# Kernel tuning notes

Hardware: AMD Instinct MI355X
Metric: run time of the kernel (lower is better)

## Reference

```python
import jax, jax.numpy as jnp
import numpy as np

N, T, D, H = 16, 1024, 1024, 1024


def setup_inputs() -> dict:
    key = jax.random.key(0)
    ks = jax.random.split(key, 7)
    x = jax.random.normal(ks[0], (N, T, D), dtype=jnp.float32)
    reset = jax.random.randint(ks[1], (N, T), 0, 2).astype(bool)
    carry = jax.random.normal(ks[2], (N, T, H), dtype=jnp.float32)
    # learned parameters (orthogonal-ish init approximated by scaled gaussian)
    initial_h = jax.random.normal(ks[3], (H,), dtype=jnp.float32) * 0.1
    w_i = jax.random.normal(ks[4], (D, 3 * H), dtype=jnp.float32) * (1.0 / np.sqrt(D))
    w_h = jax.random.normal(ks[5], (H, 3 * H), dtype=jnp.float32) * (1.0 / np.sqrt(H))
    b = jnp.zeros((3 * H,), dtype=jnp.float32)
    return {"x": x, "reset": reset, "carry": carry,
            "initial_h": initial_h, "w_i": w_i, "w_h": w_h, "b": b}


def _gru_scan(x, reset, carry, initial_h, w_i, w_h, b):
    n, t, _ = x.shape
    h_dim = initial_h.shape[0]
    # learn_initial_h and not is_target: replace carry with learned init where reset
    init_b = jnp.broadcast_to(initial_h, (n, t, h_dim))
    carry = jnp.where(reset[..., None], init_b, carry)
    # precompute input projections for all timesteps (math-equivalent hoist)
    gx = jnp.einsum('ntd,dk->ntk', x, w_i)  # [N,T,3H]
    w_h_zr, w_h_a = w_h[:, :2 * h_dim], w_h[:, 2 * h_dim:]
    b_zr, b_a = b[:2 * h_dim], b[2 * h_dim:]

    def step(h, inp):
        gx_t, reset_t, carry_t = inp  # [N,3H], [N], [N,H]
        h = jnp.where(reset_t[:, None], carry_t, h)
        zr = jax.nn.sigmoid(gx_t[:, :2 * h_dim] + h @ w_h_zr + b_zr)
        z, r = zr[:, :h_dim], zr[:, h_dim:]
        a = jnp.tanh(gx_t[:, 2 * h_dim:] + (r * h) @ w_h_a + b_a)
        h_next = (1.0 - z) * h + z * a
        return h_next, h_next

    h0 = carry[:, 0, :]  # scan init is carry_seq[:1,:] per batch element
    _, hs = jax.lax.scan(step, h0, (gx.transpose(1, 0, 2), reset.T, carry.transpose(1, 0, 2)))
    states = hs.transpose(1, 0, 2)  # [N,T,H]
    return states


def reference(x, reset, carry, initial_h, w_i, w_h, b):
    states = _gru_scan(x, reset, carry, initial_h, w_i, w_h, b)
    # hk.GRU returns (next_state, next_state): outputs_seq == states_seq
    return states, states, initial_h[None, :]
```

## Files before the change

kernel.cpp:

```cpp
#include <hip/hip_runtime.h>

typedef __attribute__((ext_vector_type(8))) short s8v;
typedef __attribute__((ext_vector_type(4))) float f4v;
typedef __attribute__((ext_vector_type(4))) unsigned int u4v;
typedef unsigned long long u64;

__device__ __forceinline__ float bf2f(unsigned short u) {
    union { float f; unsigned int i; } v; v.i = ((unsigned int)u) << 16; return v.f;
}
__device__ __forceinline__ unsigned short f2bf(float f) {
    union { float f; unsigned int i; } v; v.f = f;
    unsigned int x = v.i;
    return (unsigned short)((x + 0x7fffu + ((x >> 16) & 1u)) >> 16);
}
__device__ __forceinline__ float ldf(const void* p, size_t i, int f32) {
    return f32 ? ((const float*)p)[i] : bf2f(((const unsigned short*)p)[i]);
}

__device__ __forceinline__ s8v ald16(u64* p) {
    union { s8v v; u64 u[2]; } r;
    r.u[0] = __hip_atomic_load(p,     __ATOMIC_RELAXED, __HIP_MEMORY_SCOPE_AGENT);
    r.u[1] = __hip_atomic_load(p + 1, __ATOMIC_RELAXED, __HIP_MEMORY_SCOPE_AGENT);
    return r.v;
}
__device__ __forceinline__ void pack_store64(u64* p, int lane, unsigned short val) {
    unsigned int mv = val;
    unsigned int lo = mv | (__shfl_down(mv, 16, 64) << 16);
    unsigned int hi = __shfl_down(mv, 32, 64) | (__shfl_down(mv, 48, 64) << 16);
    if (lane < 16) {
        u64 q = (u64)lo | ((u64)hi << 32);
        __hip_atomic_store(p, q, __ATOMIC_RELAXED, __HIP_MEMORY_SCOPE_AGENT);
    }
}

__device__ __forceinline__ void pollwait(int* f, int v) {
    while (__hip_atomic_load(f, __ATOMIC_RELAXED, __HIP_MEMORY_SCOPE_AGENT) < v)
        __builtin_amdgcn_s_sleep(1);
    __builtin_amdgcn_sched_barrier(0);
    asm volatile("" ::: "memory");
}

__global__ void detect_k(const unsigned short* __restrict__ xu,
                         const unsigned int* __restrict__ rw,
                         int* __restrict__ flags) {
    __shared__ int cnt;
    int tid = threadIdx.x;
    if (tid == 0) cnt = 0;
    for (int i = tid + 8; i < 528; i += 256) flags[i] = 0;
    __syncthreads();
    int bad = 0;
    for (int i = tid; i < 4096; i += 256) {
        unsigned short v = xu[i];
        int e = (v >> 7) & 0xFF;
        if (e == 0xFF || (e <= 90 && (v & 0x7FFFu) != 0)) bad++;
    }
    atomicAdd(&cnt, bad);
    __syncthreads();
    if (tid == 0) {
        flags[0] = (cnt > 16) ? 1 : 0;
        bool w01 = true, oddz = true, ones = false, b01 = true, h16 = true, fv = true;
        for (int i = 0; i < 32; ++i) {
            unsigned int w = rw[i];
            if (w > 1u) w01 = false;
            if ((i & 1) && w != 0u) oddz = false;
            if (w != 0u) ones = true;
            if ((w & 0xFFu) > 1u || ((w >> 8) & 0xFFu) > 1u ||
                ((w >> 16) & 0xFFu) > 1u || (w >> 24) > 1u) b01 = false;
            unsigned int lo = w & 0xFFFFu, hi = w >> 16;
            if (!((lo == 0u || lo == 0x3F80u) && (hi == 0u || hi == 0x3F80u))) h16 = false;
            if (!(w == 0u || w == 0x3F800000u)) fv = false;
        }
        int mode;
        if (w01 && oddz && ones) mode = 4;
        else if (w01) mode = 0;
        else if (fv) mode = 3;
        else if (h16) mode = 2;
        else if (b01) mode = 1;
        else mode = 0;
        flags[1] = mode;
    }
}

__device__ __forceinline__ int get_reset(const void* p, int mode, int idx) {
    switch (mode) {
        case 0: return ((const int*)p)[idx] != 0;
        case 1: return ((const signed char*)p)[idx] != 0;
        case 2: return ((const unsigned short*)p)[idx] != 0;
        case 3: return ((const float*)p)[idx] != 0.f;
        default: return ((const int*)p)[idx * 2] != 0;
    }
}

__device__ __forceinline__ void stage_w(const void* w, int wf32, int j0, int tid,
                                        unsigned short* lws) {
    for (int k = tid; k < 1024; k += 256) {
        #pragma unroll
        for (int g = 0; g < 3; ++g) {
            unsigned short tmp[8];
            size_t base = (size_t)k * 3072 + g * 1024 + j0;
            if (wf32) {
                const float* wf = (const float*)w;
                f4v v0 = *(const f4v*)&wf[base];
                f4v v1 = *(const f4v*)&wf[base + 4];
                #pragma unroll
                for (int r = 0; r < 4; ++r) { tmp[r] = f2bf(v0[r]); tmp[4 + r] = f2bf(v1[r]); }
            } else {
                union { u4v v; unsigned short u[8]; } cv;
                cv.v = *(const u4v*)&((const unsigned short*)w)[base];
                #pragma unroll
                for (int r = 0; r < 8; ++r) tmp[r] = cv.u[r];
            }
            #pragma unroll
            for (int r = 0; r < 8; ++r) lws[(g * 8 + r) * 1048 + k] = tmp[r];
        }
    }
}

__global__ __launch_bounds__(256, 1) void scan64_k(
    const void* __restrict__ xv, const void* __restrict__ resetv,
    const void* __restrict__ carryv, const void* __restrict__ inithv,
    const void* __restrict__ wiv, const void* __restrict__ whv,
    const void* __restrict__ biasv, void* __restrict__ outv,
    unsigned short* __restrict__ hbuf0, unsigned short* __restrict__ hbuf1,
    unsigned short* __restrict__ rbuf0, unsigned short* __restrict__ rbuf1,
    int* __restrict__ flags) {
    __shared__ __align__(16) unsigned short lws[24 * 1048];
    __shared__ __align__(16) float lpA[2 * 1024];
    __shared__ __align__(16) float lpB[1024];

    const int xf32 = flags[0];
    const int rmode = flags[1];
    int* flagA = flags + 16;
    int* flagB = flags + 272;

    const int tid = threadIdx.x;
    const int wave = tid >> 6, lane = tid & 63;
    const int c = lane & 15, q = lane >> 4;
    const int j0 = blockIdx.x * 16;
    const int an = tid & 15, jloc = tid >> 4;
    const int jg = j0 + jloc;
    const float biasZ = ldf(biasv, jg, xf32);
    const float biasR = ldf(biasv, 1024 + jg, xf32);
    const float biasA = ldf(biasv, 2048 + jg, xf32);
    const float initj = ldf(inithv, jg, xf32);
    const unsigned short initj_b = f2bf(initj);
    const int kbase = wave * 256;
    const int qidx = an * 256 + (j0 >> 2) + wave;

    s8v whZ[8], whR[8], whA[8], wiZ[8], wiR[8], wiA[8];
    #pragma unroll
    for (int p = 0; p < 2; ++p) {
        stage_w(whv, xf32, j0 + 8 * p, tid, lws);
        __syncthreads();
        if ((c >> 3) == p) {
            int cz = c & 7;
            #pragma unroll
            for (int kc = 0; kc < 8; ++kc) {
                int kk = kbase + kc * 32 + q * 8;
                whZ[kc] = *(const s8v*)&lws[cz * 1048 + kk];
                whR[kc] = *(const s8v*)&lws[(8 + cz) * 1048 + kk];
                whA[kc] = *(const s8v*)&lws[(16 + cz) * 1048 + kk];
            }
        }
        __syncthreads();
    }
    #pragma unroll
    for (int p = 0; p < 2; ++p) {
        stage_w(wiv, xf32, j0 + 8 * p, tid, lws);
        __syncthreads();
        if ((c >> 3) == p) {
            int cz = c & 7;
            #pragma unroll
            for (int kc = 0; kc < 8; ++kc) {
                int kk = kbase + kc * 32 + q * 8;
                wiZ[kc] = *(const s8v*)&lws[cz * 1048 + kk];
                wiR[kc] = *(const s8v*)&lws[(8 + cz) * 1048 + kk];
                wiA[kc] = *(const s8v*)&lws[(16 + cz) * 1048 + kk];
            }
        }
        __syncthreads();
    }

    s8v xa[8];
    auto load_xa = [&](int tt) {
        if (xf32) {
            const float* xf = (const float*)xv;
            #pragma unroll
            for (int kc = 0; kc < 8; ++kc) {
                size_t b = (size_t)c * 1048576 + (size_t)tt * 1024 + kbase + kc * 32 + q * 8;
                f4v v0 = *(const f4v*)&xf[b];
                f4v v1 = *(const f4v*)&xf[b + 4];
                union { s8v v; unsigned short u[8]; } cv;
                #pragma unroll
                for (int r = 0; r < 4; ++r) { cv.u[r] = f2bf(v0[r]); cv.u[4 + r] = f2bf(v1[r]); }
                xa[kc] = cv.v;
            }
        } else {
            const unsigned short* xu = (const unsigned short*)xv;
            #pragma unroll
            for (int kc = 0; kc < 8; ++kc) {
                size_t b = (size_t)c * 1048576 + (size_t)tt * 1024 + kbase + kc * 32 + q * 8;
                xa[kc] = *(const s8v*)&xu[b];
            }
        }
    };

    float hreg, zreg = 0.f, he_own = 0.f;
    int rs_cur = get_reset(resetv, rmode, an * 1024);
    {
        float h0 = rs_cur ? initj : ldf(carryv, (size_t)an * 1048576 + jg, xf32);
        unsigned short hb0 = f2bf(h0);
        hreg = bf2f(hb0);
        pack_store64((u64*)hbuf0 + qidx, lane, hb0);
        if (an == 0) {
            if (xf32) ((float*)outv)[(size_t)33554432 + jg] = initj;
            else ((unsigned short*)outv)[(size_t)33554432 + jg] = initj_b;
        }
        asm volatile("s_waitcnt vmcnt(0)" ::: "memory");
        if (lane == 0)
            __hip_atomic_store(&flagB[blockIdx.x * 4 + wave], 1,
                               __ATOMIC_RELAXED, __HIP_MEMORY_SCOPE_AGENT);
    }
    load_xa(0);

    for (int t = 0; t < 1024; ++t) {
        unsigned short* hcur = (t & 1) ? hbuf1 : hbuf0;
        unsigned short* hnxt = (t & 1) ? hbuf0 : hbuf1;
        unsigned short* rcur = (t & 1) ? rbuf1 : rbuf0;

        he_own = rs_cur ? initj : hreg;
        int rs_next = (t < 1023) ? get_reset(resetv, rmode, an * 1024 + t + 1) : 0;

        f4v accZ = (f4v){0.f, 0.f, 0.f, 0.f};
        f4v accR = (f4v){0.f, 0.f, 0.f, 0.f};
        #pragma unroll
        for (int kc = 0; kc < 8; ++kc) {
            accZ = __builtin_amdgcn_mfma_f32_16x16x32_bf16(xa[kc], wiZ[kc], accZ, 0, 0, 0);
            accR = __builtin_amdgcn_mfma_f32_16x16x32_bf16(xa[kc], wiR[kc], accR, 0, 0, 0);
        }
        pollwait(&flagB[tid], t + 1);
        s8v ha[8];
        #pragma unroll
        for (int kc = 0; kc < 8; ++kc)
            ha[kc] = ald16((u64*)hcur + ((c * 1024 + kbase + kc * 32 + q * 8) >> 2));
        #pragma unroll
        for (int kc = 0; kc < 8; ++kc) {
            accZ = __builtin_amdgcn_mfma_f32_16x16x32_bf16(ha[kc], whZ[kc], accZ, 0, 0, 0);
            accR = __builtin_amdgcn_mfma_f32_16x16x32_bf16(ha[kc], whR[kc], accR, 0, 0, 0);
        }
        *(f4v*)&lpA[wave * 256 + c * 16 + q * 4] = accZ;
        *(f4v*)&lpA[1024 + wave * 256 + c * 16 + q * 4] = accR;
        __syncthreads();
        {
            float zpre = lpA[jloc * 16 + an] + lpA[256 + jloc * 16 + an] +
                         lpA[512 + jloc * 16 + an] + lpA[768 + jloc * 16 + an] + biasZ;
            float rpre = lpA[1024 + jloc * 16 + an] + lpA[1280 + jloc * 16 + an] +
                         lpA[1536 + jloc * 16 + an] + lpA[1792 + jloc * 16 + an] + biasR;
            zreg = 1.f / (1.f + expf(-zpre));
            float rg = 1.f / (1.f + expf(-rpre));
            pack_store64((u64*)rcur + qidx, lane, f2bf(rg * he_own));
            asm volatile("s_waitcnt vmcnt(0)" ::: "memory");
            if (lane == 0)
                __hip_atomic_store(&flagA[blockIdx.x * 4 + wave], t + 1,
                                   __ATOMIC_RELAXED, __HIP_MEMORY_SCOPE_AGENT);
        }

        f4v acc2 = (f4v){0.f, 0.f, 0.f, 0.f};
        #pragma unroll
        for (int kc = 0; kc < 8; ++kc)
            acc2 = __builtin_amdgcn_mfma_f32_16x16x32_bf16(xa[kc], wiA[kc], acc2, 0, 0, 0);
        pollwait(&flagA[tid], t + 1);
        s8v ra[8];
        #pragma unroll
        for (int kc = 0; kc < 8; ++kc)
            ra[kc] = ald16((u64*)rcur + ((c * 1024 + kbase + kc * 32 + q * 8) >> 2));
        #pragma unroll
        for (int kc = 0; kc < 8; ++kc)
            acc2 = __builtin_amdgcn_mfma_f32_16x16x32_bf16(ra[kc], whA[kc], acc2, 0, 0, 0);
        *(f4v*)&lpB[wave * 256 + c * 16 + q * 4] = acc2;
        __syncthreads();
        {
            float preB = lpB[jloc * 16 + an] + lpB[256 + jloc * 16 + an] +
                         lpB[512 + jloc * 16 + an] + lpB[768 + jloc * 16 + an] + biasA;
            float aa = tanhf(preB);
            float hn = (1.f - zreg) * he_own + zreg * aa;
            unsigned short hb = f2bf(hn);
            hreg = hn;
            pack_store64((u64*)hnxt + qidx, lane, rs_next ? initj_b : hb);
            asm volatile("s_waitcnt vmcnt(0)" ::: "memory");
            if (lane == 0)
                __hip_atomic_store(&flagB[blockIdx.x * 4 + wave], t + 2,
                                   __ATOMIC_RELAXED, __HIP_MEMORY_SCOPE_AGENT);
            size_t oidx = ((size_t)an * 1024 + t) * 1024 + jg;
            if (xf32) {
                float* o = (float*)outv;
                o[oidx] = hn;
                o[16777216 + oidx] = hn;
            } else {
                unsigned short* o = (unsigned short*)outv;
                o[oidx] = hb;
                o[16777216 + oidx] = hb;
            }
            rs_cur = rs_next;
        }
        if (t < 1023) load_xa(t + 1);
    }

    if (blockIdx.x == 0) {
        pollwait(&flagB[tid], 1025);
        __syncthreads();
        if (tid == 0)
            __hip_atomic_store(&flags[8], 1,
                               __ATOMIC_RELAXED, __HIP_MEMORY_SCOPE_AGENT);
    }
}

__global__ __launch_bounds__(256) void scan_fb(
    const void* __restrict__ xv, const void* __restrict__ resetv,
    const void* __restrict__ carryv, const void* __restrict__ inithv,
    const void* __restrict__ wiv, const void* __restrict__ whv,
    const void* __restrict__ biasv, void* __restrict__ outv,
    unsigned short* __restrict__ hbuf0, unsigned short* __restrict__ hbuf1,
    unsigned short* __restrict__ rbuf0, unsigned short* __restrict__ rbuf1,
    int* __restrict__ flags) {
    if (__hip_atomic_load(&flags[8], __ATOMIC_RELAXED,
                          __HIP_MEMORY_SCOPE_AGENT) != 0) return;

    __shared__ __align__(16) unsigned short lws[24 * 1048];
    __shared__ __align__(16) float lpartA[4 * 256];
    __shared__ __align__(16) float lpartB[4 * 256];
    __shared__ float lhe[128];

    const int xf32 = flags[0];
    const int rmode = flags[1];
    int* flagA = flags + 16;
    int* flagB = flags + 272;

    const int tid = threadIdx.x;
    const int wave = tid >> 6, lane = tid & 63;
    const int c = lane & 15, q = lane >> 4;
    const int j0 = blockIdx.x * 8;
    const int an = tid & 15, ac = tid >> 4;
    const int jloc = ac & 7, jg = j0 + jloc;
    const bool owner = (ac < 8);
    const int colA = owner ? jg : (1024 + jg);
    const int colB = 2048 + jg;
    const float biasA = ldf(biasv, colA, xf32);
    const float biasB = ldf(biasv, colB, xf32);
    const float initj = ldf(inithv, jg, xf32);
    const unsigned short initj_b = f2bf(initj);
    const int kbase = wave * 256;
    const int qidx = an * 256 + (j0 >> 2) + (wave & 1);

    s8v whA[8], whB[8], wiA[8], wiB[8];
    stage_w(whv, xf32, j0, tid, lws);
    __syncthreads();
    #pragma unroll
    for (int kc = 0; kc < 8; ++kc) {
        int kk = kbase + kc * 32 + q * 8;
        whA[kc] = *(const s8v*)&lws[c * 1048 + kk];
        whB[kc] = *(const s8v*)&lws[(16 + (c & 7)) * 1048 + kk];
    }
    __syncthreads();
    stage_w(wiv, xf32, j0, tid, lws);
    __syncthreads();
    #pragma unroll
    for (int kc = 0; kc < 8; ++kc) {
        int kk = kbase + kc * 32 + q * 8;
        wiA[kc] = *(const s8v*)&lws[c * 1048 + kk];
        wiB[kc] = *(const s8v*)&lws[(16 + (c & 7)) * 1048 + kk];
    }

    s8v xa[8];
    auto load_xa = [&](int tt) {
        if (xf32) {
            const float* xf = (const float*)xv;
            #pragma unroll
            for (int kc = 0; kc < 8; ++kc) {
                size_t b = (size_t)c * 1048576 + (size_t)tt * 1024 + kbase + kc * 32 + q * 8;
                f4v v0 = *(const f4v*)&xf[b];
                f4v v1 = *(const f4v*)&xf[b + 4];
                union { s8v v; unsigned short u[8]; } cv;
                #pragma unroll
                for (int r = 0; r < 4; ++r) { cv.u[r] = f2bf(v0[r]); cv.u[4 + r] = f2bf(v1[r]); }
                xa[kc] = cv.v;
            }
        } else {
            const unsigned short* xu = (const unsigned short*)xv;
            #pragma unroll
            for (int kc = 0; kc < 8; ++kc) {
                size_t b = (size_t)c * 1048576 + (size_t)tt * 1024 + kbase + kc * 32 + q * 8;
                xa[kc] = *(const s8v*)&xu[b];
            }
        }
    };

    float hreg = 0.f, zreg = 0.f, he_own = 0.f;
    int rs_cur = 0;
    if (owner) {
        rs_cur = get_reset(resetv, rmode, an * 1024);
        float h0 = rs_cur ? initj : ldf(carryv, (size_t)an * 1048576 + jg, xf32);
        unsigned short hb0 = f2bf(h0);
        hreg = bf2f(hb0);
        pack_store64((u64*)hbuf0 + qidx, lane, hb0);
        if (an == 0) {
            if (xf32) ((float*)outv)[(size_t)33554432 + jg] = initj;
            else ((unsigned short*)outv)[(size_t)33554432 + jg] = initj_b;
        }
        asm volatile("s_waitcnt vmcnt(0)" ::: "memory");
        if (lane == 0)
            __hip_atomic_store(&flagB[blockIdx.x * 2 + wave], 1,
                               __ATOMIC_RELAXED, __HIP_MEMORY_SCOPE_AGENT);
    }
    load_xa(0);

    for (int t = 0; t < 1024; ++t) {
        unsigned short* hcur = (t & 1) ? hbuf1 : hbuf0;
        unsigned short* hnxt = (t & 1) ? hbuf0 : hbuf1;
        unsigned short* rcur = (t & 1) ? rbuf1 : rbuf0;

        int rs_next = 0;
        if (owner) {
            he_own = rs_cur ? initj : hreg;
            lhe[an * 8 + jloc] = he_own;
            if (t < 1023) rs_next = get_reset(resetv, rmode, an * 1024 + t + 1);
        }

        f4v acc = (f4v){0.f, 0.f, 0.f, 0.f};
        #pragma unroll
        for (int kc = 0; kc < 8; ++kc)
            acc = __builtin_amdgcn_mfma_f32_16x16x32_bf16(xa[kc], wiA[kc], acc, 0, 0, 0);

        pollwait(&flagB[tid], t + 1);
        s8v ha[8];
        #pragma unroll
        for (int kc = 0; kc < 8; ++kc)
            ha[kc] = ald16((u64*)hcur + ((c * 1024 + kbase + kc * 32 + q * 8) >> 2));
        #pragma unroll
        for (int kc = 0; kc < 8; ++kc)
            acc = __builtin_amdgcn_mfma_f32_16x16x32_bf16(ha[kc], whA[kc], acc, 0, 0, 0);
        *(f4v*)&lpartA[wave * 256 + c * 16 + q * 4] = acc;
        __syncthreads();
        {
            float pre = lpartA[ac * 16 + an] + lpartA[256 + ac * 16 + an] +
                        lpartA[512 + ac * 16 + an] + lpartA[768 + ac * 16 + an] + biasA;
            float sg = 1.f / (1.f + expf(-pre));
            if (owner) zreg = sg;
            else {
                pack_store64((u64*)rcur + qidx, lane, f2bf(sg * lhe[an * 8 + jloc]));
                asm volatile("s_waitcnt vmcnt(0)" ::: "memory");
                if (lane == 0)
                    __hip_atomic_store(&flagA[blockIdx.x * 2 + (wave - 2)], t + 1,
                                       __ATOMIC_RELAXED, __HIP_MEMORY_SCOPE_AGENT);
            }
        }

        f4v acc2 = (f4v){0.f, 0.f, 0.f, 0.f};
        #pragma unroll
        for (int kc = 0; kc < 8; ++kc)
            acc2 = __builtin_amdgcn_mfma_f32_16x16x32_bf16(xa[kc], wiB[kc], acc2, 0, 0, 0);

        pollwait(&flagA[tid], t + 1);
        s8v ra[8];
        #pragma unroll
        for (int kc = 0; kc < 8; ++kc)
            ra[kc] = ald16((u64*)rcur + ((c * 1024 + kbase + kc * 32 + q * 8) >> 2));
        #pragma unroll
        for (int kc = 0; kc < 8; ++kc)
            acc2 = __builtin_amdgcn_mfma_f32_16x16x32_bf16(ra[kc], whB[kc], acc2, 0, 0, 0);
        *(f4v*)&lpartB[wave * 256 + c * 16 + q * 4] = acc2;
        __syncthreads();
        if (owner) {
            float preB = lpartB[ac * 16 + an] + lpartB[256 + ac * 16 + an] +
                         lpartB[512 + ac * 16 + an] + lpartB[768 + ac * 16 + an] + biasB;
            float aa = tanhf(preB);
            float hn = (1.f - zreg) * he_own + zreg * aa;
            unsigned short hb = f2bf(hn);
            hreg = hn;
            pack_store64((u64*)hnxt + qidx, lane, rs_next ? initj_b : hb);
            asm volatile("s_waitcnt vmcnt(0)" ::: "memory");
            if (lane == 0)
                __hip_atomic_store(&flagB[blockIdx.x * 2 + wave], t + 2,
                                   __ATOMIC_RELAXED, __HIP_MEMORY_SCOPE_AGENT);
            size_t oidx = ((size_t)an * 1024 + t) * 1024 + jg;
            if (xf32) {
                float* o = (float*)outv;
                o[oidx] = hn;
                o[16777216 + oidx] = hn;
            } else {
                unsigned short* o = (unsigned short*)outv;
                o[oidx] = hb;
                o[16777216 + oidx] = hb;
            }
            rs_cur = rs_next;
        }
        if (t < 1023) load_xa(t + 1);
    }
}

extern "C" void kernel_launch(void* const* d_in, const int* in_sizes, int n_in,
                              void* d_out, int out_size, void* d_ws, size_t ws_size,
                              hipStream_t stream) {
    const void* x     = d_in[0];
    const void* reset = d_in[1];
    const void* carry = d_in[2];
    const void* inith = d_in[3];
    const void* w_i   = d_in[4];
    const void* w_h   = d_in[5];
    const void* bias  = d_in[6];

    char* ws = (char*)d_ws;
    unsigned short* hbuf0 = (unsigned short*)ws;
    unsigned short* hbuf1 = (unsigned short*)(ws + 32768);
    unsigned short* rbuf0 = (unsigned short*)(ws + 65536);
    unsigned short* rbuf1 = (unsigned short*)(ws + 98304);
    int*            flags = (int*)(ws + 131072);

    detect_k<<<dim3(1), dim3(256), 0, stream>>>(
        (const unsigned short*)x, (const unsigned int*)reset, flags);

    void* kargs[] = { (void*)&x, (void*)&reset, (void*)&carry, (void*)&inith,
                      (void*)&w_i, (void*)&w_h, (void*)&bias, (void*)&d_out,
                      (void*)&hbuf0, (void*)&hbuf1, (void*)&rbuf0, (void*)&rbuf1,
                      (void*)&flags };

    hipError_t e64 = hipLaunchCooperativeKernel(
        reinterpret_cast<const void*>(&scan64_k),
        dim3(64), dim3(256), kargs, 0, stream);
    (void)e64;

    hipError_t efb = hipLaunchCooperativeKernel(
        reinterpret_cast<const void*>(&scan_fb),
        dim3(128), dim3(256), kargs, 0, stream);
    (void)efb;

    (void)in_sizes; (void)n_in; (void)out_size; (void)ws_size;
}
```

Measured before the change: 15.39 ms.

## Split GRU scan across 128 blocks with two batch-half groups

The persistent cooperative scan kernel now uses 128 blocks that each own 8 hidden columns instead of 16, with the batch split into two groups of 8 and separate flags per group. Waves are split so half compute the z gate and half the r gate, and the input projection is fused into the same MFMA accumulation chain. Each group can proceed as soon as its own flags arrive, which is meant to spread the per-step work over more CUs and overlap the two halves. In exchange, half of each MFMA's rows are zero padding, there are more global flag polls and barriers per step, and cross-block synchronisation traffic grows.

```diff
diff --git a/kernel.cpp b/kernel.cpp
--- a/kernel.cpp
+++ b/kernel.cpp
@@ -23,14 +23,18 @@
     r.u[1] = __hip_atomic_load(p + 1, __ATOMIC_RELAXED, __HIP_MEMORY_SCOPE_AGENT);
     return r.v;
 }
-__device__ __forceinline__ void pack_store64(u64* p, int lane, unsigned short val) {
+__device__ __forceinline__ void pack_store64p(u64* p, int lane, unsigned short val,
+                                              bool do_store) {
     unsigned int mv = val;
     unsigned int lo = mv | (__shfl_down(mv, 16, 64) << 16);
     unsigned int hi = __shfl_down(mv, 32, 64) | (__shfl_down(mv, 48, 64) << 16);
-    if (lane < 16) {
+    if (lane < 16 && do_store) {
         u64 q = (u64)lo | ((u64)hi << 32);
         __hip_atomic_store(p, q, __ATOMIC_RELAXED, __HIP_MEMORY_SCOPE_AGENT);
     }
+}
+__device__ __forceinline__ void pack_store64(u64* p, int lane, unsigned short val) {
+    pack_store64p(p, lane, val, true);
 }
 
 __device__ __forceinline__ void pollwait(int* f, int v) {
@@ -46,7 +50,7 @@
     __shared__ int cnt;
     int tid = threadIdx.x;
     if (tid == 0) cnt = 0;
-    for (int i = tid + 8; i < 528; i += 256) flags[i] = 0;
+    for (int i = tid + 8; i < 1040; i += 256) flags[i] = 0;
     __syncthreads();
     int bad = 0;
     for (int i = tid; i < 4096; i += 256) {
@@ -116,7 +120,7 @@
     }
 }
 
-__global__ __launch_bounds__(256, 1) void scan64_k(
+__global__ __launch_bounds__(256, 1) void scan2g_k(
     const void* __restrict__ xv, const void* __restrict__ resetv,
     const void* __restrict__ carryv, const void* __restrict__ inithv,
     const void* __restrict__ wiv, const void* __restrict__ whv,
@@ -125,89 +129,89 @@
     unsigned short* __restrict__ rbuf0, unsigned short* __restrict__ rbuf1,
     int* __restrict__ flags) {
     __shared__ __align__(16) unsigned short lws[24 * 1048];
-    __shared__ __align__(16) float lpA[2 * 1024];
-    __shared__ __align__(16) float lpB[1024];
+    float* lpA = (float*)lws;
+    float* lpB = (float*)lws + 2048;
+    float* lhe = (float*)lws + 4096;
 
     const int xf32 = flags[0];
     const int rmode = flags[1];
-    int* flagA = flags + 16;
-    int* flagB = flags + 272;
+    int* fA[2] = { flags + 16,  flags + 272 };
+    int* fB[2] = { flags + 528, flags + 784 };
 
     const int tid = threadIdx.x;
     const int wave = tid >> 6, lane = tid & 63;
     const int c = lane & 15, q = lane >> 4;
-    const int j0 = blockIdx.x * 16;
-    const int an = tid & 15, jloc = tid >> 4;
-    const int jg = j0 + jloc;
-    const float biasZ = ldf(biasv, jg, xf32);
-    const float biasR = ldf(biasv, 1024 + jg, xf32);
-    const float biasA = ldf(biasv, 2048 + jg, xf32);
+    const bool c8 = (c < 8);
+    const int j0 = blockIdx.x * 8;
+    const int an = tid & 15, ac = tid >> 4;
+    const int jloc = ac & 7, jg = j0 + jloc;
+    const bool owner = (ac < 8);
+    const int colA = owner ? jg : (1024 + jg);
+    const int colB = 2048 + jg;
+    const float biasA = ldf(biasv, colA, xf32);
+    const float biasB = ldf(biasv, colB, xf32);
     const float initj = ldf(inithv, jg, xf32);
     const unsigned short initj_b = f2bf(initj);
     const int kbase = wave * 256;
-    const int qidx = an * 256 + (j0 >> 2) + wave;
-
-    s8v whZ[8], whR[8], whA[8], wiZ[8], wiR[8], wiA[8];
+    const int qidx = an * 256 + (j0 >> 2) + (wave & 1);
+
+    s8v zero8;
+    { union { s8v v; u64 u[2]; } z; z.u[0] = 0; z.u[1] = 0; zero8 = z.v; }
+
+    s8v whA[8], whB[8], wiA[8], wiB[8];
+    stage_w(whv, xf32, j0, tid, lws);
+    __syncthreads();
     #pragma unroll
-    for (int p = 0; p < 2; ++p) {
-        stage_w(whv, xf32, j0 + 8 * p, tid, lws);
-        __syncthreads();
-        if ((c >> 3) == p) {
-            int cz = c & 7;
-            #pragma unroll
-            for (int kc = 0; kc < 8; ++kc) {
-                int kk = kbase + kc * 32 + q * 8;
-                whZ[kc] = *(const s8v*)&lws[cz * 1048 + kk];
-                whR[kc] = *(const s8v*)&lws[(8 + cz) * 1048 + kk];
-                whA[kc] = *(const s8v*)&lws[(16 + cz) * 1048 + kk];
-            }
-        }
-        __syncthreads();
-    }
+    for (int kc = 0; kc < 8; ++kc) {
+        int kk = kbase + kc * 32 + q * 8;
+        whA[kc] = *(const s8v*)&lws[c * 1048 + kk];
+        whB[kc] = *(const s8v*)&lws[(16 + (c & 7)) * 1048 + kk];
+    }
+    __syncthreads();
+    stage_w(wiv, xf32, j0, tid, lws);
+    __syncthreads();
     #pragma unroll
-    for (int p = 0; p < 2; ++p) {
-        stage_w(wiv, xf32, j0 + 8 * p, tid, lws);
-        __syncthreads();
-        if ((c >> 3) == p) {
-            int cz = c & 7;
-            #pragma unroll
-            for (int kc = 0; kc < 8; ++kc) {
-                int kk = kbase + kc * 32 + q * 8;
-                wiZ[kc] = *(const s8v*)&lws[cz * 1048 + kk];
-                wiR[kc] = *(const s8v*)&lws[(8 + cz) * 1048 + kk];
-                wiA[kc] = *(const s8v*)&lws[(16 + cz) * 1048 + kk];
-            }
-        }
-        __syncthreads();
-    }
-
-    s8v xa[8];
-    auto load_xa = [&](int tt) {
-        if (xf32) {
-            const float* xf = (const float*)xv;
-            #pragma unroll
-            for (int kc = 0; kc < 8; ++kc) {
-                size_t b = (size_t)c * 1048576 + (size_t)tt * 1024 + kbase + kc * 32 + q * 8;
-                f4v v0 = *(const f4v*)&xf[b];
-                f4v v1 = *(const f4v*)&xf[b + 4];
-                union { s8v v; unsigned short u[8]; } cv;
+    for (int kc = 0; kc < 8; ++kc) {
+        int kk = kbase + kc * 32 + q * 8;
+        wiA[kc] = *(const s8v*)&lws[c * 1048 + kk];
+        wiB[kc] = *(const s8v*)&lws[(16 + (c & 7)) * 1048 + kk];
+    }
+    __syncthreads();
+
+    s8v xa0[8], xa1[8];
+    #pragma unroll
+    for (int kc = 0; kc < 8; ++kc) { xa0[kc] = zero8; xa1[kc] = zero8; }
+    auto load_x2 = [&](int tt) {
+        if (!c8) return;
+        #pragma unroll
+        for (int g = 0; g < 2; ++g) {
+            s8v* xg = g ? xa1 : xa0;
+            size_t row = (size_t)(g * 8 + c) * 1048576 + (size_t)tt * 1024;
+            if (xf32) {
+                const float* xf = (const float*)xv;
                 #pragma unroll
-                for (int r = 0; r < 4; ++r) { cv.u[r] = f2bf(v0[r]); cv.u[4 + r] = f2bf(v1[r]); }
-                xa[kc] = cv.v;
-            }
-        } else {
-            const unsigned short* xu = (const unsigned short*)xv;
-            #pragma unroll
-            for (int kc = 0; kc < 8; ++kc) {
-                size_t b = (size_t)c * 1048576 + (size_t)tt * 1024 + kbase + kc * 32 + q * 8;
-                xa[kc] = *(const s8v*)&xu[b];
+                for (int kc = 0; kc < 8; ++kc) {
+                    size_t b = row + kbase + kc * 32 + q * 8;
+                    f4v v0 = *(const f4v*)&xf[b];
+                    f4v v1 = *(const f4v*)&xf[b + 4];
+                    union { s8v v; unsigned short u[8]; } cv;
+                    #pragma unroll
+                    for (int r = 0; r < 4; ++r) { cv.u[r] = f2bf(v0[r]); cv.u[4 + r] = f2bf(v1[r]); }
+                    xg[kc] = cv.v;
+                }
+            } else {
+                const unsigned short* xu = (const unsigned short*)xv;
+                #pragma unroll
+                for (int kc = 0; kc < 8; ++kc)
+                    xg[kc] = *(const s8v*)&xu[row + kbase + kc * 32 + q * 8];
             }
         }
     };
 
-    float hreg, zreg = 0.f, he_own = 0.f;
-    int rs_cur = get_reset(resetv, rmode, an * 1024);
-    {
+    float hreg = 0.f, zreg = 0.f, he_own = 0.f;
+    int rs_cur = 0;
+    if (owner) {
+        rs_cur = get_reset(resetv, rmode, an * 1024);
         float h0 = rs_cur ? initj : ldf(carryv, (size_t)an * 1048576 + jg, xf32);
         unsigned short hb0 = f2bf(h0);
         hreg = bf2f(hb0);
@@ -217,97 +221,117 @@
             else ((unsigned short*)outv)[(size_t)33554432 + jg] = initj_b;
         }
         asm volatile("s_waitcnt vmcnt(0)" ::: "memory");
-        if (lane == 0)
-            __hip_atomic_store(&flagB[blockIdx.x * 4 + wave], 1,
+        if (lane == 0) {
+            __hip_atomic_store(&fB[0][blockIdx.x * 2 + wave], 1,
                                __ATOMIC_RELAXED, __HIP_MEMORY_SCOPE_AGENT);
-    }
-    load_xa(0);
+            __hip_atomic_store(&fB[1][blockIdx.x * 2 + wave], 1,
+                               __ATOMIC_RELAXED, __HIP_MEMORY_SCOPE_AGENT);
+        }
+    }
+    load_x2(0);
 
     for (int t = 0; t < 1024; ++t) {
         unsigned short* hcur = (t & 1) ? hbuf1 : hbuf0;
         unsigned short* hnxt = (t & 1) ? hbuf0 : hbuf1;
         unsigned short* rcur = (t & 1) ? rbuf1 : rbuf0;
 
-        he_own = rs_cur ? initj : hreg;
-        int rs_next = (t < 1023) ? get_reset(resetv, rmode, an * 1024 + t + 1) : 0;
-
-        f4v accZ = (f4v){0.f, 0.f, 0.f, 0.f};
-        f4v accR = (f4v){0.f, 0.f, 0.f, 0.f};
-        #pragma unroll
-        for (int kc = 0; kc < 8; ++kc) {
-            accZ = __builtin_amdgcn_mfma_f32_16x16x32_bf16(xa[kc], wiZ[kc], accZ, 0, 0, 0);
-            accR = __builtin_amdgcn_mfma_f32_16x16x32_bf16(xa[kc], wiR[kc], accR, 0, 0, 0);
-        }
-        pollwait(&flagB[tid], t + 1);
-        s8v ha[8];
-        #pragma unroll
-        for (int kc = 0; kc < 8; ++kc)
-            ha[kc] = ald16((u64*)hcur + ((c * 1024 + kbase + kc * 32 + q * 8) >> 2));
-        #pragma unroll
-        for (int kc = 0; kc < 8; ++kc) {
-            accZ = __builtin_amdgcn_mfma_f32_16x16x32_bf16(ha[kc], whZ[kc], accZ, 0, 0, 0);
-            accR = __builtin_amdgcn_mfma_f32_16x16x32_bf16(ha[kc], whR[kc], accR, 0, 0, 0);
-        }
-        *(f4v*)&lpA[wave * 256 + c * 16 + q * 4] = accZ;
-        *(f4v*)&lpA[1024 + wave * 256 + c * 16 + q * 4] = accR;
-        __syncthreads();
-        {
-            float zpre = lpA[jloc * 16 + an] + lpA[256 + jloc * 16 + an] +
-                         lpA[512 + jloc * 16 + an] + lpA[768 + jloc * 16 + an] + biasZ;
-            float rpre = lpA[1024 + jloc * 16 + an] + lpA[1280 + jloc * 16 + an] +
-                         lpA[1536 + jloc * 16 + an] + lpA[1792 + jloc * 16 + an] + biasR;
-            zreg = 1.f / (1.f + expf(-zpre));
-            float rg = 1.f / (1.f + expf(-rpre));
-            pack_store64((u64*)rcur + qidx, lane, f2bf(rg * he_own));
-            asm volatile("s_waitcnt vmcnt(0)" ::: "memory");
-            if (lane == 0)
-                __hip_atomic_store(&flagA[blockIdx.x * 4 + wave], t + 1,
-                                   __ATOMIC_RELAXED, __HIP_MEMORY_SCOPE_AGENT);
-        }
-
-        f4v acc2 = (f4v){0.f, 0.f, 0.f, 0.f};
-        #pragma unroll
-        for (int kc = 0; kc < 8; ++kc)
-            acc2 = __builtin_amdgcn_mfma_f32_16x16x32_bf16(xa[kc], wiA[kc], acc2, 0, 0, 0);
-        pollwait(&flagA[tid], t + 1);
-        s8v ra[8];
-        #pragma unroll
-        for (int kc = 0; kc < 8; ++kc)
-            ra[kc] = ald16((u64*)rcur + ((c * 1024 + kbase + kc * 32 + q * 8) >> 2));
-        #pragma unroll
-        for (int kc = 0; kc < 8; ++kc)
-            acc2 = __builtin_amdgcn_mfma_f32_16x16x32_bf16(ra[kc], whA[kc], acc2, 0, 0, 0);
-        *(f4v*)&lpB[wave * 256 + c * 16 + q * 4] = acc2;
-        __syncthreads();
-        {
-            float preB = lpB[jloc * 16 + an] + lpB[256 + jloc * 16 + an] +
-                         lpB[512 + jloc * 16 + an] + lpB[768 + jloc * 16 + an] + biasA;
-            float aa = tanhf(preB);
-            float hn = (1.f - zreg) * he_own + zreg * aa;
-            unsigned short hb = f2bf(hn);
-            hreg = hn;
-            pack_store64((u64*)hnxt + qidx, lane, rs_next ? initj_b : hb);
-            asm volatile("s_waitcnt vmcnt(0)" ::: "memory");
-            if (lane == 0)
-                __hip_atomic_store(&flagB[blockIdx.x * 4 + wave], t + 2,
-                                   __ATOMIC_RELAXED, __HIP_MEMORY_SCOPE_AGENT);
-            size_t oidx = ((size_t)an * 1024 + t) * 1024 + jg;
-            if (xf32) {
-                float* o = (float*)outv;
-                o[oidx] = hn;
-                o[16777216 + oidx] = hn;
-            } else {
-                unsigned short* o = (unsigned short*)outv;
-                o[oidx] = hb;
-                o[16777216 + oidx] = hb;
-            }
-            rs_cur = rs_next;
-        }
-        if (t < 1023) load_xa(t + 1);
+        int rs_next = 0;
+        if (owner) {
+            he_own = rs_cur ? initj : hreg;
+            lhe[an * 8 + jloc] = he_own;
+            if (t < 1023) rs_next = get_reset(resetv, rmode, an * 1024 + t + 1);
+        }
+
+        #pragma unroll
+        for (int g = 0; g < 2; ++g) {
+            pollwait(&fB[g][tid], t + 1);
+            s8v ha[8];
+            #pragma unroll
+            for (int kc = 0; kc < 8; ++kc)
+                ha[kc] = c8 ? ald16((u64*)hcur +
+                          (((g * 8 + c) * 1024 + kbase + kc * 32 + q * 8) >> 2)) : zero8;
+            f4v acc = (f4v){0.f, 0.f, 0.f, 0.f};
+            #pragma unroll
+            for (int kc = 0; kc < 8; ++kc)
+                acc = __builtin_amdgcn_mfma_f32_16x16x32_bf16(ha[kc], whA[kc], acc, 0, 0, 0);
+            const s8v* xg = g ? xa1 : xa0;
+            #pragma unroll
+            for (int kc = 0; kc < 8; ++kc)
+                acc = __builtin_amdgcn_mfma_f32_16x16x32_bf16(xg[kc], wiA[kc], acc, 0, 0, 0);
+            *(f4v*)&lpA[g * 1024 + wave * 256 + c * 16 + q * 4] = acc;
+            __syncthreads();
+            {
+                int m = an & 7;
+                float pre = lpA[g * 1024 + ac * 16 + m] + lpA[g * 1024 + 256 + ac * 16 + m] +
+                            lpA[g * 1024 + 512 + ac * 16 + m] + lpA[g * 1024 + 768 + ac * 16 + m] + biasA;
+                float sg = 1.f / (1.f + expf(-pre));
+                bool gok = ((an >> 3) == g);
+                if (owner) { if (gok) zreg = sg; }
+                else {
+                    pack_store64p((u64*)rcur + qidx, lane,
+                                  f2bf(sg * lhe[an * 8 + jloc]), gok);
+                    asm volatile("s_waitcnt vmcnt(0)" ::: "memory");
+                    if (lane == 0)
+                        __hip_atomic_store(&fA[g][blockIdx.x * 2 + (wave - 2)], t + 1,
+                                           __ATOMIC_RELAXED, __HIP_MEMORY_SCOPE_AGENT);
+                }
+            }
+        }
+
+        #pragma unroll
+        for (int g = 0; g < 2; ++g) {
+            pollwait(&fA[g][tid], t + 1);
+            s8v ra[8];
+            #pragma unroll
+            for (int kc = 0; kc < 8; ++kc)
+                ra[kc] = c8 ? ald16((u64*)rcur +
+                          (((g * 8 + c) * 1024 + kbase + kc * 32 + q * 8) >> 2)) : zero8;
+            f4v acc2 = (f4v){0.f, 0.f, 0.f, 0.f};
+            #pragma unroll
+            for (int kc = 0; kc < 8; ++kc)
+                acc2 = __builtin_amdgcn_mfma_f32_16x16x32_bf16(ra[kc], whB[kc], acc2, 0, 0, 0);
+            const s8v* xg = g ? xa1 : xa0;
+            #pragma unroll
+            for (int kc = 0; kc < 8; ++kc)
+                acc2 = __builtin_amdgcn_mfma_f32_16x16x32_bf16(xg[kc], wiB[kc], acc2, 0, 0, 0);
+            *(f4v*)&lpB[g * 1024 + wave * 256 + c * 16 + q * 4] = acc2;
+            __syncthreads();
+            if (owner) {
+                bool gok = ((an >> 3) == g);
+                int m = an & 7;
+                float preB = lpB[g * 1024 + ac * 16 + m] + lpB[g * 1024 + 256 + ac * 16 + m] +
+                             lpB[g * 1024 + 512 + ac * 16 + m] + lpB[g * 1024 + 768 + ac * 16 + m] + biasB;
+                float aa = tanhf(preB);
+                float hn = (1.f - zreg) * he_own + zreg * aa;
+                unsigned short hb = f2bf(hn);
+                if (gok) hreg = hn;
+                pack_store64p((u64*)hnxt + qidx, lane,
+                              rs_next ? initj_b : hb, gok);
+                asm volatile("s_waitcnt vmcnt(0)" ::: "memory");
+                if (lane == 0)
+                    __hip_atomic_store(&fB[g][blockIdx.x * 2 + wave], t + 2,
+                                       __ATOMIC_RELAXED, __HIP_MEMORY_SCOPE_AGENT);
+                if (gok) {
+                    size_t oidx = ((size_t)an * 1024 + t) * 1024 + jg;
+                    if (xf32) {
+                        float* o = (float*)outv;
+                        o[oidx] = hn;
+                        o[16777216 + oidx] = hn;
+                    } else {
+                        unsigned short* o = (unsigned short*)outv;
+                        o[oidx] = hb;
+                        o[16777216 + oidx] = hb;
+                    }
+                }
+            }
+        }
+        if (owner) rs_cur = rs_next;
+        if (t < 1023) load_x2(t + 1);
     }
 
     if (blockIdx.x == 0) {
-        pollwait(&flagB[tid], 1025);
+        pollwait(&fB[0][tid], 1025);
+        pollwait(&fB[1][tid], 1025);
         __syncthreads();
         if (tid == 0)
             __hip_atomic_store(&flags[8], 1,
@@ -524,10 +548,10 @@
                       (void*)&hbuf0, (void*)&hbuf1, (void*)&rbuf0, (void*)&rbuf1,
                       (void*)&flags };
 
-    hipError_t e64 = hipLaunchCooperativeKernel(
-        reinterpret_cast<const void*>(&scan64_k),
-        dim3(64), dim3(256), kargs, 0, stream);
-    (void)e64;
+    hipError_t e2g = hipLaunchCooperativeKernel(
+        reinterpret_cast<const void*>(&scan2g_k),
+        dim3(128), dim3(256), kargs, 0, stream);
+    (void)e2g;
 
     hipError_t efb = hipLaunchCooperativeKernel(
         reinterpret_cast<const void*>(&scan_fb),
```

New measurement: 17.51 ms. 1.14x slower.
